# Optimization experiments

Hardware: AMD Instinct MI355X
Metric: run time of the kernel (lower is better)

## Reference

```python
import jax, jax.numpy as jnp
import numpy as np

NUM_HEADS = 16
NUM_KV_HEADS = 4
HEAD_DIM = 128
SCALE = 0.08838834764831845  # 1/sqrt(128)
BATCH = 4
SEQLEN = 1024
TOTAL = BATCH * SEQLEN


def setup_inputs() -> dict:
    key = jax.random.key(0)
    kq, kk, kv = jax.random.split(key, 3)
    q = jax.random.normal(kq, (TOTAL, NUM_HEADS, HEAD_DIM), dtype=jnp.float32)
    k = jax.random.normal(kk, (TOTAL, NUM_KV_HEADS, HEAD_DIM), dtype=jnp.float32)
    v = jax.random.normal(kv, (TOTAL, NUM_KV_HEADS, HEAD_DIM), dtype=jnp.float32)
    cu = jnp.arange(BATCH + 1, dtype=jnp.int32) * SEQLEN  # [0,1024,2048,3072,4096]
    return {"q": q, "k": k, "v": v, "cu_seqlens_q": cu, "cu_seqlens_k": cu}


def reference(q, k, v, cu_seqlens_q, cu_seqlens_k):
    # Prefill varlen causal attention (block_tables=None, empty kv cache).
    # Equal-length segments -> reshape packed tokens to [B, S, H, D].
    B = cu_seqlens_q.shape[0] - 1
    S = q.shape[0] // B
    H, Dh = q.shape[1], q.shape[2]
    Hkv = k.shape[1]
    g = H // Hkv  # GQA group size

    qb = q.reshape(B, S, H, Dh)
    # repeat_interleave kv heads to match query heads
    kb = jnp.repeat(k.reshape(B, S, Hkv, Dh), g, axis=2)  # [B,S,H,Dh]
    vb = jnp.repeat(v.reshape(B, S, Hkv, Dh), g, axis=2)

    scores = jnp.einsum('bqhd,bkhd->bhqk', qb, kb) * SCALE  # [B,H,S,S]
    causal = jnp.tril(jnp.ones((S, S), dtype=bool))
    scores = jnp.where(causal, scores, jnp.finfo(scores.dtype).min)
    probs = jax.nn.softmax(scores, axis=-1)
    o = jnp.einsum('bhqk,bkhd->bqhd', probs, vb)  # [B,S,H,Dh]
    return o.reshape(B * S, H, Dh)
```

## Files before the change

kernel.cpp:

```cpp
#include <hip/hip_runtime.h>
#include <hip/hip_bf16.h>
#include <cstddef>

#define NH 16
#define NKV 4
#define HD 128
#define SEQ 1024
#define SCALE_F 0.08838834764831845f
#define LOG2E 1.44269504088896f

typedef __attribute__((ext_vector_type(8))) short short8;
typedef __attribute__((ext_vector_type(4))) short bshort4;
typedef __attribute__((ext_vector_type(4))) float floatx4;

union F8 { short8 v; bshort4 h[2]; unsigned short u[8]; };
union PK { bshort4 v; unsigned int u[2]; };

__device__ __forceinline__ unsigned short f2bf(float f) {
  unsigned int u = __float_as_uint(f);
  u += 0x7FFFu + ((u >> 16) & 1u);
  return (unsigned short)(u >> 16);
}

__device__ __forceinline__ unsigned int pkbf(float a, float b) {
  union { __hip_bfloat162 h; unsigned int u; } c;
  c.h = __float22bfloat162_rn(float2{a, b});
  return c.u;
}

__device__ __forceinline__ void glds16(const void* g, void* l) {
  __builtin_amdgcn_global_load_lds(
      (const __attribute__((address_space(1))) unsigned int*)g,
      (__attribute__((address_space(3))) unsigned int*)l, 16, 0, 0);
}

__global__ __launch_bounds__(256) void prepass(const float* __restrict__ kg,
                                               const float* __restrict__ vg,
                                               unsigned short* __restrict__ Ktg,
                                               unsigned short* __restrict__ Vtg) {
  __shared__ float Vl[32 * 132];
  const int tid = threadIdx.x;
  const int bid = blockIdx.x;
  if (bid < 512) {
    const int bkvh = bid >> 5, tile = bid & 31;
    const int b = bkvh >> 2, kvh = bkvh & 3;
    const int kpos = tid >> 3;
    const int d8base = (tid & 7) * 2;
    const size_t tok = (size_t)b * SEQ + tile * 32 + kpos;
    const float* src = kg + (tok * NKV + kvh) * HD + d8base * 8;
    unsigned short* dstT = Ktg + (size_t)bid * 4096;
#pragma unroll
    for (int i = 0; i < 2; ++i) {
      floatx4 a = ((const floatx4*)src)[0];
      floatx4 c = ((const floatx4*)src)[1];
      F8 t;
#pragma unroll
      for (int j = 0; j < 4; ++j) { t.u[j] = f2bf(a[j]); t.u[4 + j] = f2bf(c[j]); }
      const int blk = kpos * 16 + ((d8base + i) ^ (kpos & 15));
      *(short8*)(dstT + blk * 8) = t.v;
      src += 8;
    }
  } else {
    const int bb = bid - 512;
    const int bkvh = bb >> 5, tile = bb & 31;
    const int b = bkvh >> 2, kvh = bkvh & 3;
    const int r = tid >> 3;
    const int c16 = (tid & 7) * 16;
    const size_t tok = (size_t)b * SEQ + tile * 32 + r;
    const float* src = vg + (tok * NKV + kvh) * HD + c16;
#pragma unroll
    for (int j = 0; j < 4; ++j)
      *(floatx4*)&Vl[r * 132 + c16 + j * 4] = ((const floatx4*)src)[j];
    __syncthreads();
    unsigned short* dstT = Vtg + (size_t)bb * 4096;
#pragma unroll
    for (int i = 0; i < 2; ++i) {
      const int s = tid * 2 + i;
      const int dt = s >> 6;
      const int rem = s & 63;
      const int col = rem >> 2;
      const int qpos = rem & 3;
      const int quad = qpos ^ (col & 3);
      F8 t;
#pragma unroll
      for (int mt = 0; mt < 2; ++mt)
#pragma unroll
        for (int j = 0; j < 4; ++j)
          t.u[mt * 4 + j] = f2bf(Vl[(mt * 16 + quad * 4 + j) * 132 + dt * 16 + col]);
      *(short8*)(dstT + s * 8) = t.v;
    }
  }
}

__global__ __launch_bounds__(128, 2)
void fa_fwd3(const float* __restrict__ qg, const unsigned short* __restrict__ Ktg,
             const unsigned short* __restrict__ Vtg, float* __restrict__ og) {
  __shared__ __align__(16) unsigned short Kb[2][4096];
  __shared__ __align__(16) unsigned short Vb[2][4096];

  const int tid = threadIdx.x;
  const int wave = tid >> 6;
  const int lane = tid & 63;
  const int col = lane & 15;
  const int quad = lane >> 4;

  const int idx = blockIdx.x;
  const int g = idx >> 8;
  const int u = (idx >> 6) & 3;
  const int bh = idx & 63;
  const int qt = g * 4 + ((u + g) & 3);
  const int h = bh & 15;
  const int b = bh >> 4;
  const int kvh = h >> 2;
  const int seg = b * SEQ;
  const int wq0 = qt * 64 + wave * 32;
  const int tb = (b * NKV + kvh) * 32;

  F8 qf[2][4];
#pragma unroll
  for (int nt = 0; nt < 2; ++nt) {
    const float* qp =
        qg + ((size_t)(seg + wq0 + nt * 16 + col) * NH + h) * HD + quad * 8;
#pragma unroll
    for (int ks = 0; ks < 4; ++ks) {
      floatx4 a = ((const floatx4*)(qp + ks * 32))[0];
      floatx4 c = ((const floatx4*)(qp + ks * 32))[1];
#pragma unroll
      for (int j = 0; j < 4; ++j) {
        qf[nt][ks].u[j] = f2bf(a[j] * (SCALE_F * LOG2E));
        qf[nt][ks].u[4 + j] = f2bf(c[j] * (SCALE_F * LOG2E));
      }
    }
  }

  floatx4 acc[2][8];
#pragma unroll
  for (int nt = 0; nt < 2; ++nt)
#pragma unroll
    for (int dt = 0; dt < 8; ++dt) acc[nt][dt] = (floatx4){0.f, 0.f, 0.f, 0.f};
  float lsum[2] = {0.f, 0.f};

  const int nkt = 2 * (qt + 1);
  const int stg = wave * 4096 + lane * 16;
  const int stl = wave * 4096;

  {
    const char* gK = (const char*)Ktg + (size_t)tb * 8192 + stg;
    const char* gV = (const char*)Vtg + (size_t)tb * 8192 + stg;
    char* lK = (char*)&Kb[0][0] + stl;
    char* lV = (char*)&Vb[0][0] + stl;
#pragma unroll
    for (int o = 0; o < 4096; o += 1024) {
      glds16(gK + o, lK + o);
      glds16(gV + o, lV + o);
    }
  }
  __syncthreads();

  for (int kt = 0; kt < nkt; ++kt) {
    const int cb = kt & 1, nb = cb ^ 1;
    if (kt + 1 < nkt) {
      const char* gK = (const char*)Ktg + (size_t)(tb + kt + 1) * 8192 + stg;
      const char* gV = (const char*)Vtg + (size_t)(tb + kt + 1) * 8192 + stg;
      char* lK = (char*)&Kb[nb][0] + stl;
      char* lV = (char*)&Vb[nb][0] + stl;
#pragma unroll
      for (int o = 0; o < 4096; o += 1024) {
        glds16(gK + o, lK + o);
        glds16(gV + o, lV + o);
      }
    }
    const int kbase = kt * 32;
    if (kbase <= wq0 + 31) {
      floatx4 st[2][2];
#pragma unroll
      for (int nt = 0; nt < 2; ++nt)
#pragma unroll
        for (int mt = 0; mt < 2; ++mt) st[nt][mt] = (floatx4){0.f, 0.f, 0.f, 0.f};
#pragma unroll
      for (int mt = 0; mt < 2; ++mt)
#pragma unroll
        for (int ks = 0; ks < 4; ++ks) {
          F8 kf;
          kf.v = *(const short8*)&Kb[cb][((mt * 16 + col) * 16 +
                                          ((ks * 4 + quad) ^ col)) * 8];
          st[0][mt] = __builtin_amdgcn_mfma_f32_16x16x32_bf16(
              kf.v, qf[0][ks].v, st[0][mt], 0, 0, 0);
          st[1][mt] = __builtin_amdgcn_mfma_f32_16x16x32_bf16(
              kf.v, qf[1][ks].v, st[1][mt], 0, 0, 0);
        }
      const bool diag = (kbase + 31 > wq0);
      PK pf[2][2];
#pragma unroll
      for (int nt = 0; nt < 2; ++nt) {
#pragma unroll
        for (int mt = 0; mt < 2; ++mt) {
          float p[4];
#pragma unroll
          for (int r = 0; r < 4; ++r) {
            p[r] = exp2f(st[nt][mt][r]);
            if (diag) {
              const int kpos_g = kbase + mt * 16 + quad * 4 + r;
              if (kpos_g > wq0 + nt * 16 + col) p[r] = 0.f;
            }
          }
          lsum[nt] += (p[0] + p[1]) + (p[2] + p[3]);
          pf[nt][mt].u[0] = pkbf(p[0], p[1]);
          pf[nt][mt].u[1] = pkbf(p[2], p[3]);
        }
      }
#pragma unroll
      for (int dt = 0; dt < 8; ++dt) {
        F8 vf;
        vf.v = *(const short8*)&Vb[cb][(dt * 64 + col * 4 +
                                        (quad ^ (col & 3))) * 8];
#pragma unroll
        for (int nt = 0; nt < 2; ++nt) {
          acc[nt][dt] = __builtin_amdgcn_mfma_f32_16x16x16bf16_1k(
              vf.h[0], pf[nt][0].v, acc[nt][dt], 0, 0, 0);
          acc[nt][dt] = __builtin_amdgcn_mfma_f32_16x16x16bf16_1k(
              vf.h[1], pf[nt][1].v, acc[nt][dt], 0, 0, 0);
        }
      }
    }
    __syncthreads();
  }

#pragma unroll
  for (int nt = 0; nt < 2; ++nt) {
    float l = lsum[nt];
    l += __shfl_xor(l, 16);
    l += __shfl_xor(l, 32);
    const float inv = 1.0f / l;
    float* op = og + ((size_t)(seg + wq0 + nt * 16 + col) * NH + h) * HD +
                quad * 4;
#pragma unroll
    for (int dt = 0; dt < 8; ++dt) {
      floatx4 o = acc[nt][dt];
      o[0] *= inv; o[1] *= inv; o[2] *= inv; o[3] *= inv;
      *(floatx4*)(op + dt * 16) = o;
    }
  }
}

#define KST 136
#define VST 40
#define PST 40

__global__ __launch_bounds__(256, 2)
void fa_fwd(const float* __restrict__ qg, const float* __restrict__ kg,
            const float* __restrict__ vg, float* __restrict__ og) {
  __shared__ unsigned short Klds[32 * KST];
  __shared__ unsigned short Vt[HD * VST];
  __shared__ unsigned short Pl[4][32 * PST];

  const int tid = threadIdx.x;
  const int wave = tid >> 6;
  const int lane = tid & 63;
  const int col = lane & 15;
  const int quad = lane >> 4;

  const int idx = blockIdx.x;
  const int raw = idx & 7;
  const int qt = (idx & 256) ? raw : 7 - raw;
  const int bh = idx >> 3;
  const int h = bh & 15;
  const int b = bh >> 4;
  const int kvh = h >> 2;
  const int seg = b * SEQ;
  const int wq0 = qt * 128 + wave * 32;

  F8 qf[2][4];
#pragma unroll
  for (int mt = 0; mt < 2; ++mt) {
    const size_t qrow = (size_t)(seg + wq0 + mt * 16 + col);
    const float* qp = qg + (qrow * NH + h) * HD + quad * 8;
#pragma unroll
    for (int ks = 0; ks < 4; ++ks) {
      const floatx4* p4 = (const floatx4*)(qp + ks * 32);
      floatx4 a = p4[0], c = p4[1];
#pragma unroll
      for (int j = 0; j < 4; ++j) {
        qf[mt][ks].u[j] = f2bf(a[j] * SCALE_F);
        qf[mt][ks].u[4 + j] = f2bf(c[j] * SCALE_F);
      }
    }
  }

  floatx4 acc[2][8];
#pragma unroll
  for (int mt = 0; mt < 2; ++mt)
#pragma unroll
    for (int dt = 0; dt < 8; ++dt)
      acc[mt][dt] = (floatx4){0.f, 0.f, 0.f, 0.f};
  float lsum[2][4];
#pragma unroll
  for (int mt = 0; mt < 2; ++mt)
#pragma unroll
    for (int r = 0; r < 4; ++r) lsum[mt][r] = 0.f;

  const int nkt = 4 * (qt + 1);
  const int sr = tid >> 3;
  const int sc = (tid & 7) * 16;

  for (int kt = 0; kt < nkt; ++kt) {
    const int kbase = kt * 32;
    __syncthreads();
    {
      const size_t tok = (size_t)(seg + kbase + sr);
      const floatx4* kp4 = (const floatx4*)(kg + (tok * NKV + kvh) * HD + sc);
      floatx4 kv0 = kp4[0], kv1 = kp4[1], kv2 = kp4[2], kv3 = kp4[3];
      float kf32[16] = {kv0[0],kv0[1],kv0[2],kv0[3], kv1[0],kv1[1],kv1[2],kv1[3],
                        kv2[0],kv2[1],kv2[2],kv2[3], kv3[0],kv3[1],kv3[2],kv3[3]};
      unsigned int* dst = (unsigned int*)&Klds[sr * KST + sc];
#pragma unroll
      for (int j = 0; j < 8; ++j)
        dst[j] = (unsigned int)f2bf(kf32[2 * j]) | ((unsigned int)f2bf(kf32[2 * j + 1]) << 16);
      const floatx4* vp4 = (const floatx4*)(vg + (tok * NKV + kvh) * HD + sc);
      floatx4 vv0 = vp4[0], vv1 = vp4[1], vv2 = vp4[2], vv3 = vp4[3];
      unsigned short vb[16] = {
        f2bf(vv0[0]),f2bf(vv0[1]),f2bf(vv0[2]),f2bf(vv0[3]),
        f2bf(vv1[0]),f2bf(vv1[1]),f2bf(vv1[2]),f2bf(vv1[3]),
        f2bf(vv2[0]),f2bf(vv2[1]),f2bf(vv2[2]),f2bf(vv2[3]),
        f2bf(vv3[0]),f2bf(vv3[1]),f2bf(vv3[2]),f2bf(vv3[3])};
#pragma unroll
      for (int s = 0; s < 16; ++s) {
        int j = (s + tid) & 15;
        Vt[(sc + j) * VST + sr] = vb[j];
      }
    }
    __syncthreads();

    if (kbase > wq0 + 31) continue;

    F8 kf[4][2];
#pragma unroll
    for (int ks = 0; ks < 4; ++ks)
#pragma unroll
      for (int nt = 0; nt < 2; ++nt)
        kf[ks][nt].v = *(const short8*)&Klds[(nt * 16 + col) * KST + ks * 32 + quad * 8];

#pragma unroll
    for (int mt = 0; mt < 2; ++mt) {
      floatx4 s0 = {0.f, 0.f, 0.f, 0.f}, s1 = {0.f, 0.f, 0.f, 0.f};
#pragma unroll
      for (int ks = 0; ks < 4; ++ks) {
        s0 = __builtin_amdgcn_mfma_f32_16x16x32_bf16(qf[mt][ks].v, kf[ks][0].v, s0, 0, 0, 0);
        s1 = __builtin_amdgcn_mfma_f32_16x16x32_bf16(qf[mt][ks].v, kf[ks][1].v, s1, 0, 0, 0);
      }
      const int q0 = wq0 + mt * 16 + quad * 4;
      const bool diag = (kbase + 31 > wq0 + mt * 16);
      unsigned short* pw = &Pl[wave][(mt * 16 + quad * 4) * PST];
#pragma unroll
      for (int r = 0; r < 4; ++r) {
        float p0 = __expf(s0[r]);
        float p1 = __expf(s1[r]);
        if (diag) {
          p0 = (kbase + col > q0 + r) ? 0.f : p0;
          p1 = (kbase + 16 + col > q0 + r) ? 0.f : p1;
        }
        lsum[mt][r] += p0 + p1;
        pw[r * PST + col] = f2bf(p0);
        pw[r * PST + 16 + col] = f2bf(p1);
      }
    }
    F8 pa[2];
#pragma unroll
    for (int mt = 0; mt < 2; ++mt)
      pa[mt].v = *(const short8*)&Pl[wave][(mt * 16 + col) * PST + quad * 8];
#pragma unroll
    for (int dt = 0; dt < 8; ++dt) {
      F8 vb;
      vb.v = *(const short8*)&Vt[(dt * 16 + col) * VST + quad * 8];
#pragma unroll
      for (int mt = 0; mt < 2; ++mt)
        acc[mt][dt] = __builtin_amdgcn_mfma_f32_16x16x32_bf16(pa[mt].v, vb.v, acc[mt][dt], 0, 0, 0);
    }
  }

#pragma unroll
  for (int mt = 0; mt < 2; ++mt) {
#pragma unroll
    for (int r = 0; r < 4; ++r) {
      float l = lsum[mt][r];
      l += __shfl_xor(l, 1);
      l += __shfl_xor(l, 2);
      l += __shfl_xor(l, 4);
      l += __shfl_xor(l, 8);
      const float inv = 1.0f / l;
      const int qi = wq0 + mt * 16 + quad * 4 + r;
      float* op = og + ((size_t)(seg + qi) * NH + h) * HD;
#pragma unroll
      for (int dt = 0; dt < 8; ++dt)
        op[dt * 16 + col] = acc[mt][dt][r] * inv;
    }
  }
}

extern "C" void kernel_launch(void* const* d_in, const int* in_sizes, int n_in,
                              void* d_out, int out_size, void* d_ws, size_t ws_size,
                              hipStream_t stream) {
  const float* q = (const float*)d_in[0];
  const float* k = (const float*)d_in[1];
  const float* v = (const float*)d_in[2];
  float* out = (float*)d_out;
  if (ws_size >= (size_t)(8 * 1024 * 1024)) {
    unsigned short* Ktg = (unsigned short*)d_ws;
    unsigned short* Vtg = Ktg + 2097152;
    hipLaunchKernelGGL(prepass, dim3(1024), dim3(256), 0, stream, k, v, Ktg, Vtg);
    hipLaunchKernelGGL(fa_fwd3, dim3(1024), dim3(128), 0, stream, q, Ktg, Vtg, out);
  } else {
    hipLaunchKernelGGL(fa_fwd, dim3(512), dim3(256), 0, stream, q, k, v, out);
  }
}
```

Measured before the change: 145.6 us.

## Split KV range across waves with 32-row query tiles and LDS reduction

The attention kernel now gives each block a 32-row query tile and splits the causal KV tiles between its two waves (even/odd), merging partial accumulators and row sums through LDS at the end. V is read straight from global into registers in a relayout matching a single 16x16x32 MFMA, and P goes through a small swizzled LDS buffer instead of being kept in registers. Each wave prefetches its own K tile independently, with waitcnt instead of block-wide barriers. The grid doubles and occupancy is raised to 4 blocks, aiming for better load balance and latency hiding. The cost is extra LDS traffic for P and the final reduction, plus uncached global V loads.

```diff
diff --git a/kernel.cpp b/kernel.cpp
--- a/kernel.cpp
+++ b/kernel.cpp
@@ -10,11 +10,10 @@
 #define LOG2E 1.44269504088896f
 
 typedef __attribute__((ext_vector_type(8))) short short8;
-typedef __attribute__((ext_vector_type(4))) short bshort4;
 typedef __attribute__((ext_vector_type(4))) float floatx4;
-
-union F8 { short8 v; bshort4 h[2]; unsigned short u[8]; };
-union PK { bshort4 v; unsigned int u[2]; };
+typedef __attribute__((ext_vector_type(2))) unsigned int uintx2;
+
+union F8 { short8 v; unsigned short u[8]; };
 
 __device__ __forceinline__ unsigned short f2bf(float f) {
   unsigned int u = __float_as_uint(f);
@@ -61,8 +60,8 @@
       src += 8;
     }
   } else {
-    const int bb = bid - 512;
-    const int bkvh = bb >> 5, tile = bb & 31;
+    const int bb2 = bid - 512;
+    const int bkvh = bb2 >> 5, tile = bb2 & 31;
     const int b = bkvh >> 2, kvh = bkvh & 3;
     const int r = tid >> 3;
     const int c16 = (tid & 7) * 16;
@@ -72,55 +71,52 @@
     for (int j = 0; j < 4; ++j)
       *(floatx4*)&Vl[r * 132 + c16 + j * 4] = ((const floatx4*)src)[j];
     __syncthreads();
-    unsigned short* dstT = Vtg + (size_t)bb * 4096;
+    unsigned short* dstT = Vtg + (size_t)bb2 * 4096;
 #pragma unroll
     for (int i = 0; i < 2; ++i) {
       const int s = tid * 2 + i;
       const int dt = s >> 6;
-      const int rem = s & 63;
-      const int col = rem >> 2;
-      const int qpos = rem & 3;
-      const int quad = qpos ^ (col & 3);
+      const int ln = s & 63;
+      const int qd = ln >> 4;
+      const int cl = ln & 15;
       F8 t;
 #pragma unroll
-      for (int mt = 0; mt < 2; ++mt)
-#pragma unroll
-        for (int j = 0; j < 4; ++j)
-          t.u[mt * 4 + j] = f2bf(Vl[(mt * 16 + quad * 4 + j) * 132 + dt * 16 + col]);
+      for (int j = 0; j < 8; ++j)
+        t.u[j] = f2bf(Vl[(qd * 8 + j) * 132 + dt * 16 + cl]);
       *(short8*)(dstT + s * 8) = t.v;
     }
   }
 }
 
-__global__ __launch_bounds__(128, 2)
-void fa_fwd3(const float* __restrict__ qg, const unsigned short* __restrict__ Ktg,
+__global__ __launch_bounds__(128, 4)
+void fa_fwd4(const float* __restrict__ qg, const unsigned short* __restrict__ Ktg,
              const unsigned short* __restrict__ Vtg, float* __restrict__ og) {
   __shared__ __align__(16) unsigned short Kb[2][4096];
-  __shared__ __align__(16) unsigned short Vb[2][4096];
+  __shared__ __align__(16) unsigned int Pbuf[2][512];
 
   const int tid = threadIdx.x;
-  const int wave = tid >> 6;
+  const int w = tid >> 6;
   const int lane = tid & 63;
   const int col = lane & 15;
   const int quad = lane >> 4;
 
   const int idx = blockIdx.x;
-  const int g = idx >> 8;
-  const int u = (idx >> 6) & 3;
-  const int bh = idx & 63;
-  const int qt = g * 4 + ((u + g) & 3);
+  const int jj = idx >> 8;
+  const int u = idx & 255;
+  const int bh = u >> 2;
+  const int qt = jj * 4 + (((u & 3) + jj) & 3);
   const int h = bh & 15;
   const int b = bh >> 4;
   const int kvh = h >> 2;
   const int seg = b * SEQ;
-  const int wq0 = qt * 64 + wave * 32;
-  const int tb = (b * NKV + kvh) * 32;
+  const int q0 = qt * 32;
+  const size_t tbase = (size_t)((b * NKV + kvh) * 32) * 8192;
 
   F8 qf[2][4];
 #pragma unroll
   for (int nt = 0; nt < 2; ++nt) {
     const float* qp =
-        qg + ((size_t)(seg + wq0 + nt * 16 + col) * NH + h) * HD + quad * 8;
+        qg + ((size_t)(seg + q0 + nt * 16 + col) * NH + h) * HD + quad * 8;
 #pragma unroll
     for (int ks = 0; ks < 4; ++ks) {
       floatx4 a = ((const floatx4*)(qp + ks * 32))[0];
@@ -140,105 +136,103 @@
     for (int dt = 0; dt < 8; ++dt) acc[nt][dt] = (floatx4){0.f, 0.f, 0.f, 0.f};
   float lsum[2] = {0.f, 0.f};
 
-  const int nkt = 2 * (qt + 1);
-  const int stg = wave * 4096 + lane * 16;
-  const int stl = wave * 4096;
-
-  {
-    const char* gK = (const char*)Ktg + (size_t)tb * 8192 + stg;
-    const char* gV = (const char*)Vtg + (size_t)tb * 8192 + stg;
-    char* lK = (char*)&Kb[0][0] + stl;
-    char* lV = (char*)&Vb[0][0] + stl;
-#pragma unroll
-    for (int o = 0; o < 4096; o += 1024) {
-      glds16(gK + o, lK + o);
-      glds16(gV + o, lV + o);
-    }
-  }
+  char* lk = (char*)&Kb[w][0];
+  if (w <= qt) {
+    const char* gk = (const char*)Ktg + tbase + (size_t)w * 8192 + lane * 16;
+#pragma unroll
+    for (int o = 0; o < 8192; o += 1024) glds16(gk + o, lk + o);
+  }
+
+  for (int p = w; p <= qt; p += 2) {
+    __builtin_amdgcn_s_waitcnt(0x0f70);
+    __builtin_amdgcn_sched_barrier(0);
+    F8 vf[8];
+    const char* vsrc = (const char*)Vtg + tbase + (size_t)p * 8192 + lane * 16;
+#pragma unroll
+    for (int dt = 0; dt < 8; ++dt) vf[dt].v = *(const short8*)(vsrc + dt * 1024);
+    floatx4 st[2][2];
+#pragma unroll
+    for (int nt = 0; nt < 2; ++nt)
+#pragma unroll
+      for (int hh = 0; hh < 2; ++hh) st[nt][hh] = (floatx4){0.f, 0.f, 0.f, 0.f};
+#pragma unroll
+    for (int hh = 0; hh < 2; ++hh)
+#pragma unroll
+      for (int ks = 0; ks < 4; ++ks) {
+        F8 kf;
+        kf.v = *(const short8*)&Kb[w][hh * 2048 +
+                                      (col * 16 + ((ks * 4 + quad) ^ col)) * 8];
+        st[0][hh] = __builtin_amdgcn_mfma_f32_16x16x32_bf16(
+            kf.v, qf[0][ks].v, st[0][hh], 0, 0, 0);
+        st[1][hh] = __builtin_amdgcn_mfma_f32_16x16x32_bf16(
+            kf.v, qf[1][ks].v, st[1][hh], 0, 0, 0);
+      }
+    const bool diag = (p == qt);
+#pragma unroll
+    for (int nt = 0; nt < 2; ++nt)
+#pragma unroll
+      for (int hh = 0; hh < 2; ++hh) {
+        float pr[4];
+#pragma unroll
+        for (int r = 0; r < 4; ++r) {
+          pr[r] = exp2f(st[nt][hh][r]);
+          if (diag && (p * 32 + hh * 16 + quad * 4 + r > q0 + nt * 16 + col))
+            pr[r] = 0.f;
+        }
+        lsum[nt] += (pr[0] + pr[1]) + (pr[2] + pr[3]);
+        const int bbi = hh * 2 + (quad >> 1);
+        unsigned int* pw = &Pbuf[w][(nt * 16 + col) * 16 +
+                                    ((bbi ^ (col & 3)) << 2) + ((quad & 1) << 1)];
+        *(uintx2*)pw = (uintx2){pkbf(pr[0], pr[1]), pkbf(pr[2], pr[3])};
+      }
+    F8 pb[2];
+#pragma unroll
+    for (int nt = 0; nt < 2; ++nt)
+      pb[nt].v = *(const short8*)&Pbuf[w][(nt * 16 + col) * 16 +
+                                          ((quad ^ (col & 3)) << 2)];
+    __builtin_amdgcn_sched_barrier(0);
+    if (p + 2 <= qt) {
+      const char* gk =
+          (const char*)Ktg + tbase + (size_t)(p + 2) * 8192 + lane * 16;
+#pragma unroll
+      for (int o = 0; o < 8192; o += 1024) glds16(gk + o, lk + o);
+    }
+#pragma unroll
+    for (int dt = 0; dt < 8; ++dt)
+#pragma unroll
+      for (int nt = 0; nt < 2; ++nt)
+        acc[nt][dt] = __builtin_amdgcn_mfma_f32_16x16x32_bf16(
+            vf[dt].v, pb[nt].v, acc[nt][dt], 0, 0, 0);
+  }
+
   __syncthreads();
-
-  for (int kt = 0; kt < nkt; ++kt) {
-    const int cb = kt & 1, nb = cb ^ 1;
-    if (kt + 1 < nkt) {
-      const char* gK = (const char*)Ktg + (size_t)(tb + kt + 1) * 8192 + stg;
-      const char* gV = (const char*)Vtg + (size_t)(tb + kt + 1) * 8192 + stg;
-      char* lK = (char*)&Kb[nb][0] + stl;
-      char* lV = (char*)&Vb[nb][0] + stl;
-#pragma unroll
-      for (int o = 0; o < 4096; o += 1024) {
-        glds16(gK + o, lK + o);
-        glds16(gV + o, lV + o);
-      }
-    }
-    const int kbase = kt * 32;
-    if (kbase <= wq0 + 31) {
-      floatx4 st[2][2];
-#pragma unroll
-      for (int nt = 0; nt < 2; ++nt)
-#pragma unroll
-        for (int mt = 0; mt < 2; ++mt) st[nt][mt] = (floatx4){0.f, 0.f, 0.f, 0.f};
-#pragma unroll
-      for (int mt = 0; mt < 2; ++mt)
-#pragma unroll
-        for (int ks = 0; ks < 4; ++ks) {
-          F8 kf;
-          kf.v = *(const short8*)&Kb[cb][((mt * 16 + col) * 16 +
-                                          ((ks * 4 + quad) ^ col)) * 8];
-          st[0][mt] = __builtin_amdgcn_mfma_f32_16x16x32_bf16(
-              kf.v, qf[0][ks].v, st[0][mt], 0, 0, 0);
-          st[1][mt] = __builtin_amdgcn_mfma_f32_16x16x32_bf16(
-              kf.v, qf[1][ks].v, st[1][mt], 0, 0, 0);
-        }
-      const bool diag = (kbase + 31 > wq0);
-      PK pf[2][2];
-#pragma unroll
-      for (int nt = 0; nt < 2; ++nt) {
-#pragma unroll
-        for (int mt = 0; mt < 2; ++mt) {
-          float p[4];
-#pragma unroll
-          for (int r = 0; r < 4; ++r) {
-            p[r] = exp2f(st[nt][mt][r]);
-            if (diag) {
-              const int kpos_g = kbase + mt * 16 + quad * 4 + r;
-              if (kpos_g > wq0 + nt * 16 + col) p[r] = 0.f;
-            }
-          }
-          lsum[nt] += (p[0] + p[1]) + (p[2] + p[3]);
-          pf[nt][mt].u[0] = pkbf(p[0], p[1]);
-          pf[nt][mt].u[1] = pkbf(p[2], p[3]);
-        }
-      }
+  float* cb = (float*)&Kb[0][0];
+  float* lb = (float*)&Pbuf[0][0];
+  if (w == 1) {
+#pragma unroll
+    for (int nt = 0; nt < 2; ++nt)
+#pragma unroll
+      for (int dt = 0; dt < 8; ++dt)
+        *(floatx4*)&cb[((nt * 8 + dt) * 64 + lane) * 4] = acc[nt][dt];
+    lb[lane] = lsum[0];
+    lb[64 + lane] = lsum[1];
+  }
+  __syncthreads();
+  if (w == 0) {
+#pragma unroll
+    for (int nt = 0; nt < 2; ++nt) {
+      float l = lsum[nt] + lb[nt * 64 + lane];
+      l += __shfl_xor(l, 16);
+      l += __shfl_xor(l, 32);
+      const float inv = 1.0f / l;
+      float* op = og + ((size_t)(seg + q0 + nt * 16 + col) * NH + h) * HD +
+                  quad * 4;
 #pragma unroll
       for (int dt = 0; dt < 8; ++dt) {
-        F8 vf;
-        vf.v = *(const short8*)&Vb[cb][(dt * 64 + col * 4 +
-                                        (quad ^ (col & 3))) * 8];
-#pragma unroll
-        for (int nt = 0; nt < 2; ++nt) {
-          acc[nt][dt] = __builtin_amdgcn_mfma_f32_16x16x16bf16_1k(
-              vf.h[0], pf[nt][0].v, acc[nt][dt], 0, 0, 0);
-          acc[nt][dt] = __builtin_amdgcn_mfma_f32_16x16x16bf16_1k(
-              vf.h[1], pf[nt][1].v, acc[nt][dt], 0, 0, 0);
-        }
-      }
-    }
-    __syncthreads();
-  }
-
-#pragma unroll
-  for (int nt = 0; nt < 2; ++nt) {
-    float l = lsum[nt];
-    l += __shfl_xor(l, 16);
-    l += __shfl_xor(l, 32);
-    const float inv = 1.0f / l;
-    float* op = og + ((size_t)(seg + wq0 + nt * 16 + col) * NH + h) * HD +
-                quad * 4;
-#pragma unroll
-    for (int dt = 0; dt < 8; ++dt) {
-      floatx4 o = acc[nt][dt];
-      o[0] *= inv; o[1] *= inv; o[2] *= inv; o[3] *= inv;
-      *(floatx4*)(op + dt * 16) = o;
+        floatx4 o = acc[nt][dt] + *(const floatx4*)&cb[((nt * 8 + dt) * 64 + lane) * 4];
+        o[0] *= inv; o[1] *= inv; o[2] *= inv; o[3] *= inv;
+        *(floatx4*)(op + dt * 16) = o;
+      }
     }
   }
 }
@@ -408,7 +402,7 @@
     unsigned short* Ktg = (unsigned short*)d_ws;
     unsigned short* Vtg = Ktg + 2097152;
     hipLaunchKernelGGL(prepass, dim3(1024), dim3(256), 0, stream, k, v, Ktg, Vtg);
-    hipLaunchKernelGGL(fa_fwd3, dim3(1024), dim3(128), 0, stream, q, Ktg, Vtg, out);
+    hipLaunchKernelGGL(fa_fwd4, dim3(2048), dim3(128), 0, stream, q, Ktg, Vtg, out);
   } else {
     hipLaunchKernelGGL(fa_fwd, dim3(512), dim3(256), 0, stream, q, k, v, out);
   }
```

After: 265.8 us. +82.5%, slower.
